# Performance work log

Hardware: AMD Instinct MI355X
Metric: run time of the kernel (lower is better)

The kernel has to match this reference:

```python
import jax, jax.numpy as jnp
import numpy as np

N_NODES = 100000
H = 256
E = 500000

def setup_inputs() -> dict:
    key = jax.random.key(0)
    ks = jax.random.split(key, 7)
    z_src = jax.random.normal(ks[0], (N_NODES, H), dtype=jnp.float32)
    z_dst = jax.random.normal(ks[1], (N_NODES, H), dtype=jnp.float32)
    edge_label_index = jax.random.randint(ks[2], (2, E), 0, N_NODES, dtype=jnp.int64)
    # Linear params, scaled like torch default init (~1/sqrt(fan_in))
    w1 = jax.random.normal(ks[3], (H, 2 * H), dtype=jnp.float32) * (1.0 / np.sqrt(2 * H))
    b1 = jax.random.normal(ks[4], (H,), dtype=jnp.float32) * (1.0 / np.sqrt(2 * H))
    w2 = jax.random.normal(ks[5], (1, H), dtype=jnp.float32) * (1.0 / np.sqrt(H))
    b2 = jax.random.normal(ks[6], (1,), dtype=jnp.float32) * (1.0 / np.sqrt(H))
    return {"z_src": z_src, "z_dst": z_dst, "edge_label_index": edge_label_index,
            "w1": w1, "b1": b1, "w2": w2, "b2": b2}

def reference(z_src, z_dst, edge_label_index, w1, b1, w2, b2):
    row, col = edge_label_index[0], edge_label_index[1]
    # gather edge endpoint features and concat -> [E, 2H]
    z = jnp.concatenate([z_src[row], z_dst[col]], axis=-1)
    z = jax.nn.relu(jnp.einsum('eh,oh->eo', z, w1) + b1)  # [E, H]
    z = jnp.einsum('eh,oh->eo', z, w2) + b2               # [E, 1]
    return jax.nn.sigmoid(z).reshape(-1)
```

## Files before the change

kernel.cpp:

```cpp
#include <hip/hip_runtime.h>

#define E_TOT 500000
#define N_NODES 100000
#define NUNITS_H 3125

typedef __attribute__((ext_vector_type(16))) float f32x16;
typedef __attribute__((ext_vector_type(8))) short short8;
typedef __attribute__((ext_vector_type(4))) float f32x4;

__device__ __forceinline__ unsigned short f2bf(float f) {
  union { float f; unsigned u; } x; x.f = f;
  unsigned r = x.u + 0x7fffu + ((x.u >> 16) & 1u);
  return (unsigned short)(r >> 16);
}

__device__ __forceinline__ float bf2f(unsigned short s) {
  union { unsigned u; float f; } x; x.u = ((unsigned)s) << 16;
  return x.f;
}

__global__ void k_repack_w1h(const float* __restrict__ w1,
                             unsigned short* __restrict__ w1r2) {
  int o = blockIdx.x * 256 + threadIdx.x;
  int half = o >> 16;
  int kb = (o >> 11) & 31;
  int n = (o >> 3) & 255;
  int j = o & 7;
  w1r2[o] = f2bf(w1[n * 512 + half * 256 + kb * 8 + j]);
}

__global__ __launch_bounds__(512, 2) void k_node_gemm(
    const float* __restrict__ zsrc, const float* __restrict__ zdst,
    const unsigned short* __restrict__ w1r2, const float* __restrict__ b1,
    unsigned short* __restrict__ Uo, unsigned short* __restrict__ Vo) {
  __shared__ __align__(16) unsigned short Ap[2][8192];
  __shared__ __align__(16) unsigned short Ct[2][8192];

  const int half = blockIdx.x >> 7;
  const int bh = blockIdx.x & 127;
  const float* Z = half ? zdst : zsrc;
  unsigned short* O = half ? Vo : Uo;

  const unsigned tid = threadIdx.x;
  const unsigned l = tid & 63u;
  const unsigned wv = tid >> 6;
  const unsigned l31 = l & 31u;
  const unsigned hi = l >> 5;
  const unsigned arow = tid & 31u;
  const unsigned ak2 = tid >> 5;

  short8 brg[16];
  {
    const unsigned short* bb = w1r2 + (unsigned)half * 65536u;
#pragma unroll
    for (int k = 0; k < 16; ++k) {
      unsigned ks = (unsigned)k * 2u + hi;
      brg[k] = *(const short8*)(bb + (ks * 256u + wv * 32u + l31) * 8u);
      asm volatile("" : "+v"(brg[k]));
    }
  }

  const float bi = half ? 0.f : b1[wv * 32u + l31];

  f32x4 ap[4];
#define LOAD_A(uu)                                                        \
  {                                                                       \
    const f32x4* p_ =                                                     \
        (const f32x4*)(Z + ((long)(uu)*32 + arow) * 256 + ak2 * 16u);     \
    ap[0] = p_[0]; ap[1] = p_[1]; ap[2] = p_[2]; ap[3] = p_[3];           \
  }
#define WRITE_A(bf_)                                                      \
  {                                                                       \
    _Pragma("unroll") for (int g = 0; g < 2; ++g) {                       \
      short8 sa;                                                          \
      sa[0] = (short)f2bf(ap[2*g].x);   sa[1] = (short)f2bf(ap[2*g].y);   \
      sa[2] = (short)f2bf(ap[2*g].z);   sa[3] = (short)f2bf(ap[2*g].w);   \
      sa[4] = (short)f2bf(ap[2*g+1].x); sa[5] = (short)f2bf(ap[2*g+1].y); \
      sa[6] = (short)f2bf(ap[2*g+1].z); sa[7] = (short)f2bf(ap[2*g+1].w); \
      *(short8*)&Ap[bf_][((2u*ak2 + (unsigned)g)*32u + arow)*8u] = sa;    \
    }                                                                     \
  }

  int u = bh;
  int cur = 0;
  LOAD_A(u);
  WRITE_A(0);
  __syncthreads();

  for (; u < NUNITS_H; u += 128) {
    int un = u + 128;
    if (un >= NUNITS_H) un = u;
    LOAD_A(un);
    __builtin_amdgcn_sched_barrier(0);

    f32x16 acc = {0.f, 0.f, 0.f, 0.f, 0.f, 0.f, 0.f, 0.f,
                  0.f, 0.f, 0.f, 0.f, 0.f, 0.f, 0.f, 0.f};
#pragma unroll
    for (int kk = 0; kk < 16; ++kk) {
      unsigned ks = 2u * (unsigned)kk + hi;
      short8 af = *(const short8*)&Ap[cur][(ks * 32u + l31) * 8u];
      acc = __builtin_amdgcn_mfma_f32_32x32x16_bf16(af, brg[kk], acc, 0, 0, 0);
    }

#pragma unroll
    for (int r = 0; r < 16; ++r) {
      unsigned row32 = (unsigned)((r & 3) + 8 * (r >> 2)) + 4u * hi;
      Ct[cur][row32 * 256u + wv * 32u + l31] = f2bf(acc[r] + bi);
    }
    WRITE_A(cur ^ 1);
    __syncthreads();

    {
      const long gbase = (long)u * 32 * 256;
#pragma unroll
      for (int p = 0; p < 2; ++p) {
        unsigned s = (unsigned)p * 512u + tid;
        unsigned row = s >> 5;
        unsigned seg = s & 31u;
        short8 vv = *(const short8*)&Ct[cur][row * 256u + seg * 8u];
        *(short8*)(O + gbase + row * 256u + seg * 8u) = vv;
      }
    }
    cur ^= 1;
  }
#undef LOAD_A
#undef WRITE_A
}

#define EK_ITER 16
__global__ __launch_bounds__(256, 6) void k_edge(
    const unsigned short* __restrict__ U, const unsigned short* __restrict__ V,
    const int* __restrict__ eli, const float* __restrict__ w2,
    const float* __restrict__ b2, float* __restrict__ out) {
  const int tid = threadIdx.x;
  const int g = tid >> 4;
  const int j = tid & 15;
  float w2v[16];
#pragma unroll
  for (int q = 0; q < 8; ++q) {
    w2v[q] = w2[8 * j + q];
    w2v[8 + q] = w2[128 + 8 * j + q];
  }
  const float b2v = b2[0];
  const long base = (long)blockIdx.x * (16 * EK_ITER) + g;

#define CLAMP_E(k) \
  (((base + 16 * (k)) < E_TOT) ? (base + 16 * (k)) : (long)(E_TOT - 1))

  long eP = CLAMP_E(0);
  int rA = eli[eP], cA = eli[E_TOT + eP];
  long eQ = CLAMP_E(1);
  int rB = eli[eQ], cB = eli[E_TOT + eQ];
  short8 uA0 = *(const short8*)(U + (long)rA * 256 + 8 * j);
  short8 uA1 = *(const short8*)(U + (long)rA * 256 + 128 + 8 * j);
  short8 vA0 = *(const short8*)(V + (long)cA * 256 + 8 * j);
  short8 vA1 = *(const short8*)(V + (long)cA * 256 + 128 + 8 * j);
  short8 uB0, uB1, vB0, vB1;

#pragma unroll
  for (int it2 = 0; it2 < EK_ITER / 2; ++it2) {
    {
      long eN = CLAMP_E(2 * it2 + 2);
      int rN = eli[eN], cN = eli[E_TOT + eN];
      uB0 = *(const short8*)(U + (long)rB * 256 + 8 * j);
      uB1 = *(const short8*)(U + (long)rB * 256 + 128 + 8 * j);
      vB0 = *(const short8*)(V + (long)cB * 256 + 8 * j);
      vB1 = *(const short8*)(V + (long)cB * 256 + 128 + 8 * j);
      rB = rN; cB = cN;
      float p = 0.f;
#pragma unroll
      for (int q = 0; q < 8; ++q) {
        float a0 = bf2f((unsigned short)uA0[q]) + bf2f((unsigned short)vA0[q]);
        float a1 = bf2f((unsigned short)uA1[q]) + bf2f((unsigned short)vA1[q]);
        p = fmaf(fmaxf(a0, 0.f), w2v[q], p);
        p = fmaf(fmaxf(a1, 0.f), w2v[8 + q], p);
      }
      p += __shfl_xor(p, 1);
      p += __shfl_xor(p, 2);
      p += __shfl_xor(p, 4);
      p += __shfl_xor(p, 8);
      long e = base + 16 * (2 * it2);
      if (j == 0 && e < E_TOT) out[e] = 1.f / (1.f + __expf(-(p + b2v)));
    }
    {
      long eN = CLAMP_E(2 * it2 + 3);
      int rN = eli[eN], cN = eli[E_TOT + eN];
      uA0 = *(const short8*)(U + (long)rB * 256 + 8 * j);
      uA1 = *(const short8*)(U + (long)rB * 256 + 128 + 8 * j);
      vA0 = *(const short8*)(V + (long)cB * 256 + 8 * j);
      vA1 = *(const short8*)(V + (long)cB * 256 + 128 + 8 * j);
      rB = rN; cB = cN;
      float p = 0.f;
#pragma unroll
      for (int q = 0; q < 8; ++q) {
        float a0 = bf2f((unsigned short)uB0[q]) + bf2f((unsigned short)vB0[q]);
        float a1 = bf2f((unsigned short)uB1[q]) + bf2f((unsigned short)vB1[q]);
        p = fmaf(fmaxf(a0, 0.f), w2v[q], p);
        p = fmaf(fmaxf(a1, 0.f), w2v[8 + q], p);
      }
      p += __shfl_xor(p, 1);
      p += __shfl_xor(p, 2);
      p += __shfl_xor(p, 4);
      p += __shfl_xor(p, 8);
      long e = base + 16 * (2 * it2 + 1);
      if (j == 0 && e < E_TOT) out[e] = 1.f / (1.f + __expf(-(p + b2v)));
    }
  }
#undef CLAMP_E
}

extern "C" void kernel_launch(void* const* d_in, const int* in_sizes, int n_in,
                              void* d_out, int out_size, void* d_ws,
                              size_t ws_size, hipStream_t stream) {
  const float* zsrc = (const float*)d_in[0];
  const float* zdst = (const float*)d_in[1];
  const int* eli = (const int*)d_in[2];
  const float* w1 = (const float*)d_in[3];
  const float* b1 = (const float*)d_in[4];
  const float* w2 = (const float*)d_in[5];
  const float* b2 = (const float*)d_in[6];
  float* out = (float*)d_out;

  const size_t uv_bytes = (size_t)N_NODES * 256 * 2;
  unsigned short* U = (unsigned short*)d_ws;
  unsigned short* V = (unsigned short*)((char*)d_ws + uv_bytes);
  unsigned short* w1r2 = (unsigned short*)((char*)d_ws + 2 * uv_bytes);

  k_repack_w1h<<<512, 256, 0, stream>>>(w1, w1r2);
  k_node_gemm<<<256, 512, 0, stream>>>(zsrc, zdst, w1r2, b1, U, V);
  int nbe = (E_TOT + 16 * EK_ITER - 1) / (16 * EK_ITER);
  k_edge<<<nbe, 256, 0, stream>>>(U, V, eli, w2, b2, out);
}
```

Baseline: 149.1 us.

## Deepen node GEMM prefetch to three register buffers for A tiles

Reworks the node GEMM main loop so global loads of the fp32 input tiles are issued three iterations ahead, rotating through three register buffer sets instead of one. Launch bounds drop to one block per CU to make room for the extra registers. The goal is to hide more HBM latency on the streaming read of z_src/z_dst, at the cost of lower occupancy and higher register pressure.

```diff
diff --git a/kernel.cpp b/kernel.cpp
--- a/kernel.cpp
+++ b/kernel.cpp
@@ -3,6 +3,7 @@
 #define E_TOT 500000
 #define N_NODES 100000
 #define NUNITS_H 3125
+#define SRD 128
 
 typedef __attribute__((ext_vector_type(16))) float f32x16;
 typedef __attribute__((ext_vector_type(8))) short short8;
@@ -29,7 +30,7 @@
   w1r2[o] = f2bf(w1[n * 512 + half * 256 + kb * 8 + j]);
 }
 
-__global__ __launch_bounds__(512, 2) void k_node_gemm(
+__global__ __launch_bounds__(512, 1) void k_node_gemm(
     const float* __restrict__ zsrc, const float* __restrict__ zdst,
     const unsigned short* __restrict__ w1r2, const float* __restrict__ b1,
     unsigned short* __restrict__ Uo, unsigned short* __restrict__ Vo) {
@@ -62,67 +63,76 @@
 
   const float bi = half ? 0.f : b1[wv * 32u + l31];
 
-  f32x4 ap[4];
-#define LOAD_A(uu)                                                        \
+  f32x4 apA[4], apB[4], apC[4];
+
+#define LOAD_A(uu, ap_)                                                   \
   {                                                                       \
+    int uc_ = (uu); if (uc_ >= NUNITS_H) uc_ = NUNITS_H - 1;              \
     const f32x4* p_ =                                                     \
-        (const f32x4*)(Z + ((long)(uu)*32 + arow) * 256 + ak2 * 16u);     \
-    ap[0] = p_[0]; ap[1] = p_[1]; ap[2] = p_[2]; ap[3] = p_[3];           \
-  }
-#define WRITE_A(bf_)                                                      \
+        (const f32x4*)(Z + ((long)uc_ * 32 + arow) * 256 + ak2 * 16u);    \
+    ap_[0] = p_[0]; ap_[1] = p_[1]; ap_[2] = p_[2]; ap_[3] = p_[3];       \
+  }
+#define WRITE_A(ap_, bf_)                                                 \
   {                                                                       \
     _Pragma("unroll") for (int g = 0; g < 2; ++g) {                       \
       short8 sa;                                                          \
-      sa[0] = (short)f2bf(ap[2*g].x);   sa[1] = (short)f2bf(ap[2*g].y);   \
-      sa[2] = (short)f2bf(ap[2*g].z);   sa[3] = (short)f2bf(ap[2*g].w);   \
-      sa[4] = (short)f2bf(ap[2*g+1].x); sa[5] = (short)f2bf(ap[2*g+1].y); \
-      sa[6] = (short)f2bf(ap[2*g+1].z); sa[7] = (short)f2bf(ap[2*g+1].w); \
+      sa[0] = (short)f2bf(ap_[2*g].x);   sa[1] = (short)f2bf(ap_[2*g].y); \
+      sa[2] = (short)f2bf(ap_[2*g].z);   sa[3] = (short)f2bf(ap_[2*g].w); \
+      sa[4] = (short)f2bf(ap_[2*g+1].x); sa[5] = (short)f2bf(ap_[2*g+1].y); \
+      sa[6] = (short)f2bf(ap_[2*g+1].z); sa[7] = (short)f2bf(ap_[2*g+1].w); \
       *(short8*)&Ap[bf_][((2u*ak2 + (unsigned)g)*32u + arow)*8u] = sa;    \
     }                                                                     \
+  }
+
+#define BODY(uu, NEW, WR)                                                 \
+  {                                                                       \
+    LOAD_A((uu) + 3 * SRD, NEW);                                          \
+    __builtin_amdgcn_sched_barrier(0);                                    \
+    f32x16 acc = {0.f, 0.f, 0.f, 0.f, 0.f, 0.f, 0.f, 0.f,                 \
+                  0.f, 0.f, 0.f, 0.f, 0.f, 0.f, 0.f, 0.f};                \
+    _Pragma("unroll") for (int kk = 0; kk < 16; ++kk) {                   \
+      unsigned ks = 2u * (unsigned)kk + hi;                               \
+      short8 af = *(const short8*)&Ap[cur][(ks * 32u + l31) * 8u];        \
+      acc = __builtin_amdgcn_mfma_f32_32x32x16_bf16(af, brg[kk], acc, 0, 0, 0); \
+    }                                                                     \
+    _Pragma("unroll") for (int r = 0; r < 16; ++r) {                      \
+      unsigned row32 = (unsigned)((r & 3) + 8 * (r >> 2)) + 4u * hi;      \
+      Ct[cur][row32 * 256u + wv * 32u + l31] = f2bf(acc[r] + bi);         \
+    }                                                                     \
+    WRITE_A(WR, cur ^ 1);                                                 \
+    __syncthreads();                                                      \
+    {                                                                     \
+      const long gbase = (long)(uu) * 32 * 256;                           \
+      _Pragma("unroll") for (int p = 0; p < 2; ++p) {                     \
+        unsigned s = (unsigned)p * 512u + tid;                            \
+        unsigned row = s >> 5;                                            \
+        unsigned seg = s & 31u;                                           \
+        short8 vv = *(const short8*)&Ct[cur][row * 256u + seg * 8u];      \
+        *(short8*)(O + gbase + row * 256u + seg * 8u) = vv;               \
+      }                                                                   \
+    }                                                                     \
+    cur ^= 1;                                                             \
   }
 
   int u = bh;
   int cur = 0;
-  LOAD_A(u);
-  WRITE_A(0);
+  LOAD_A(u, apA);
+  WRITE_A(apA, 0);
+  LOAD_A(u + SRD, apB);
+  LOAD_A(u + 2 * SRD, apC);
   __syncthreads();
 
-  for (; u < NUNITS_H; u += 128) {
-    int un = u + 128;
-    if (un >= NUNITS_H) un = u;
-    LOAD_A(un);
-    __builtin_amdgcn_sched_barrier(0);
-
-    f32x16 acc = {0.f, 0.f, 0.f, 0.f, 0.f, 0.f, 0.f, 0.f,
-                  0.f, 0.f, 0.f, 0.f, 0.f, 0.f, 0.f, 0.f};
-#pragma unroll
-    for (int kk = 0; kk < 16; ++kk) {
-      unsigned ks = 2u * (unsigned)kk + hi;
-      short8 af = *(const short8*)&Ap[cur][(ks * 32u + l31) * 8u];
-      acc = __builtin_amdgcn_mfma_f32_32x32x16_bf16(af, brg[kk], acc, 0, 0, 0);
-    }
-
-#pragma unroll
-    for (int r = 0; r < 16; ++r) {
-      unsigned row32 = (unsigned)((r & 3) + 8 * (r >> 2)) + 4u * hi;
-      Ct[cur][row32 * 256u + wv * 32u + l31] = f2bf(acc[r] + bi);
-    }
-    WRITE_A(cur ^ 1);
-    __syncthreads();
-
-    {
-      const long gbase = (long)u * 32 * 256;
-#pragma unroll
-      for (int p = 0; p < 2; ++p) {
-        unsigned s = (unsigned)p * 512u + tid;
-        unsigned row = s >> 5;
-        unsigned seg = s & 31u;
-        short8 vv = *(const short8*)&Ct[cur][row * 256u + seg * 8u];
-        *(short8*)(O + gbase + row * 256u + seg * 8u) = vv;
-      }
-    }
-    cur ^= 1;
-  }
+  for (; u < NUNITS_H;) {
+    BODY(u, apA, apB);
+    u += SRD;
+    if (u >= NUNITS_H) break;
+    BODY(u, apB, apC);
+    u += SRD;
+    if (u >= NUNITS_H) break;
+    BODY(u, apC, apA);
+    u += SRD;
+  }
+#undef BODY
 #undef LOAD_A
 #undef WRITE_A
 }
```

Result: faster. 143.1 us (-4.0%).

## Stage fp32 node features into LDS via direct global-to-LDS loads with XOR swizzle

Applied to the files above, without the earlier changes.

The node GEMM kernel now copies fp32 feature tiles straight from global memory into a swizzled LDS buffer using global_load_lds, instead of loading into registers, converting to bf16 and writing LDS. The bf16 conversion moves to LDS read time just before each MFMA, and the grid doubles to 512 blocks with a single output staging buffer and an extra barrier. The aim is to cut register pressure and VALU work in the load path and raise memory-level parallelism. In exchange, LDS traffic doubles because fp32 is staged, LDS use grows to 80KB per block, which may limit blocks per CU, and each iteration gains an additional barrier.

```diff
diff --git a/kernel.cpp b/kernel.cpp
--- a/kernel.cpp
+++ b/kernel.cpp
@@ -1,8 +1,10 @@
 #include <hip/hip_runtime.h>
+#include <hip/hip_bf16.h>
 
 #define E_TOT 500000
 #define N_NODES 100000
 #define NUNITS_H 3125
+#define SRD 256
 
 typedef __attribute__((ext_vector_type(16))) float f32x16;
 typedef __attribute__((ext_vector_type(8))) short short8;
@@ -17,6 +19,18 @@
 __device__ __forceinline__ float bf2f(unsigned short s) {
   union { unsigned u; float f; } x; x.u = ((unsigned)s) << 16;
   return x.f;
+}
+
+__device__ __forceinline__ short cvt1(float f) {
+  __hip_bfloat16 h = __float2bfloat16(f);
+  union { __hip_bfloat16 h; short s; } u; u.h = h;
+  return u.s;
+}
+
+__device__ __forceinline__ void gl_lds16(const void* g, void* l) {
+  __builtin_amdgcn_global_load_lds(
+      (const __attribute__((address_space(1))) void*)g,
+      (__attribute__((address_space(3))) void*)l, 16, 0, 0);
 }
 
 __global__ void k_repack_w1h(const float* __restrict__ w1,
@@ -33,11 +47,11 @@
     const float* __restrict__ zsrc, const float* __restrict__ zdst,
     const unsigned short* __restrict__ w1r2, const float* __restrict__ b1,
     unsigned short* __restrict__ Uo, unsigned short* __restrict__ Vo) {
-  __shared__ __align__(16) unsigned short Ap[2][8192];
-  __shared__ __align__(16) unsigned short Ct[2][8192];
-
-  const int half = blockIdx.x >> 7;
-  const int bh = blockIdx.x & 127;
+  __shared__ __align__(16) char smem[81920];
+  unsigned short* Ct = (unsigned short*)(smem + 65536);
+
+  const int half = blockIdx.x >> 8;
+  const int bh = blockIdx.x & 255;
   const float* Z = half ? zdst : zsrc;
   unsigned short* O = half ? Vo : Uo;
 
@@ -46,8 +60,7 @@
   const unsigned wv = tid >> 6;
   const unsigned l31 = l & 31u;
   const unsigned hi = l >> 5;
-  const unsigned arow = tid & 31u;
-  const unsigned ak2 = tid >> 5;
+  const unsigned xr = (l31 & 7u) << 4;
 
   short8 brg[16];
   {
@@ -62,53 +75,52 @@
 
   const float bi = half ? 0.f : b1[wv * 32u + l31];
 
-  f32x4 ap[4];
-#define LOAD_A(uu)                                                        \
+#define STAGE(uu, bf)                                                     \
   {                                                                       \
-    const f32x4* p_ =                                                     \
-        (const f32x4*)(Z + ((long)(uu)*32 + arow) * 256 + ak2 * 16u);     \
-    ap[0] = p_[0]; ap[1] = p_[1]; ap[2] = p_[2]; ap[3] = p_[3];           \
-  }
-#define WRITE_A(bf_)                                                      \
-  {                                                                       \
-    _Pragma("unroll") for (int g = 0; g < 2; ++g) {                       \
-      short8 sa;                                                          \
-      sa[0] = (short)f2bf(ap[2*g].x);   sa[1] = (short)f2bf(ap[2*g].y);   \
-      sa[2] = (short)f2bf(ap[2*g].z);   sa[3] = (short)f2bf(ap[2*g].w);   \
-      sa[4] = (short)f2bf(ap[2*g+1].x); sa[5] = (short)f2bf(ap[2*g+1].y); \
-      sa[6] = (short)f2bf(ap[2*g+1].z); sa[7] = (short)f2bf(ap[2*g+1].w); \
-      *(short8*)&Ap[bf_][((2u*ak2 + (unsigned)g)*32u + arow)*8u] = sa;    \
+    int uc_ = (uu); if (uc_ >= NUNITS_H) uc_ = NUNITS_H - 1;              \
+    const char* src_ = (const char*)(Z + (long)uc_ * 32 * 256);           \
+    char* dst_ = smem + (unsigned)(bf)*32768u;                            \
+    _Pragma("unroll") for (int q = 0; q < 4; ++q) {                       \
+      unsigned row_ = wv * 4u + (unsigned)q;                              \
+      unsigned off_ = row_ * 1024u;                                       \
+      unsigned so_ = off_ + ((l * 16u) ^ ((row_ & 7u) << 4));             \
+      gl_lds16(src_ + so_, dst_ + off_);                                  \
     }                                                                     \
   }
 
   int u = bh;
   int cur = 0;
-  LOAD_A(u);
-  WRITE_A(0);
-  __syncthreads();
-
-  for (; u < NUNITS_H; u += 128) {
-    int un = u + 128;
-    if (un >= NUNITS_H) un = u;
-    LOAD_A(un);
+  STAGE(u, 0);
+  asm volatile("s_waitcnt vmcnt(0)" ::: "memory");
+  __builtin_amdgcn_s_barrier();
+
+  for (; u < NUNITS_H; u += SRD) {
+    STAGE(u + SRD, cur ^ 1);
     __builtin_amdgcn_sched_barrier(0);
 
+    const char* Ab = smem + (unsigned)cur * 32768u;
     f32x16 acc = {0.f, 0.f, 0.f, 0.f, 0.f, 0.f, 0.f, 0.f,
                   0.f, 0.f, 0.f, 0.f, 0.f, 0.f, 0.f, 0.f};
 #pragma unroll
     for (int kk = 0; kk < 16; ++kk) {
-      unsigned ks = 2u * (unsigned)kk + hi;
-      short8 af = *(const short8*)&Ap[cur][(ks * 32u + l31) * 8u];
+      unsigned c0 = (unsigned)kk * 64u + hi * 32u;
+      f32x4 a0 = *(const f32x4*)(Ab + l31 * 1024u + (c0 ^ xr));
+      f32x4 a1 = *(const f32x4*)(Ab + l31 * 1024u + ((c0 + 16u) ^ xr));
+      short8 af;
+      af[0] = cvt1(a0.x); af[1] = cvt1(a0.y);
+      af[2] = cvt1(a0.z); af[3] = cvt1(a0.w);
+      af[4] = cvt1(a1.x); af[5] = cvt1(a1.y);
+      af[6] = cvt1(a1.z); af[7] = cvt1(a1.w);
       acc = __builtin_amdgcn_mfma_f32_32x32x16_bf16(af, brg[kk], acc, 0, 0, 0);
     }
 
 #pragma unroll
     for (int r = 0; r < 16; ++r) {
       unsigned row32 = (unsigned)((r & 3) + 8 * (r >> 2)) + 4u * hi;
-      Ct[cur][row32 * 256u + wv * 32u + l31] = f2bf(acc[r] + bi);
-    }
-    WRITE_A(cur ^ 1);
-    __syncthreads();
+      Ct[row32 * 256u + wv * 32u + l31] = f2bf(acc[r] + bi);
+    }
+    asm volatile("s_waitcnt vmcnt(0) lgkmcnt(0)" ::: "memory");
+    __builtin_amdgcn_s_barrier();
 
     {
       const long gbase = (long)u * 32 * 256;
@@ -117,14 +129,14 @@
         unsigned s = (unsigned)p * 512u + tid;
         unsigned row = s >> 5;
         unsigned seg = s & 31u;
-        short8 vv = *(const short8*)&Ct[cur][row * 256u + seg * 8u];
+        short8 vv = *(const short8*)&Ct[row * 256u + seg * 8u];
         *(short8*)(O + gbase + row * 256u + seg * 8u) = vv;
       }
     }
+    __builtin_amdgcn_s_barrier();
     cur ^= 1;
   }
-#undef LOAD_A
-#undef WRITE_A
+#undef STAGE
 }
 
 #define EK_ITER 16
@@ -227,7 +239,7 @@
   unsigned short* w1r2 = (unsigned short*)((char*)d_ws + 2 * uv_bytes);
 
   k_repack_w1h<<<512, 256, 0, stream>>>(w1, w1r2);
-  k_node_gemm<<<256, 512, 0, stream>>>(zsrc, zdst, w1r2, b1, U, V);
+  k_node_gemm<<<512, 512, 0, stream>>>(zsrc, zdst, w1r2, b1, U, V);
   int nbe = (E_TOT + 16 * EK_ITER - 1) / (16 * EK_ITER);
   k_edge<<<nbe, 256, 0, stream>>>(U, V, eli, w2, b2, out);
 }
```

Measured after the change: 139.4 us. 6.5% less time.
